# Kernel optimization log

Measured on AMD Instinct MI355X. Metric: run time of the kernel, lower is better.

## Reference

```python
import jax, jax.numpy as jnp
import numpy as np

E = 16      # number of encoders
L = 3       # RNN blocks per encoder
D_IN = 32   # input feature dim
D = 512     # RNN state dim
H_FF = 2048 # encoder FFNN hidden
D_ENC = 512 # encoder output dim
N_DEC = 4   # decoder layers
H_DEC = 2048
D_OUT = 1024
T = 128     # sequence length


def setup_inputs() -> dict:
    key = jax.random.key(0)
    ks = jax.random.split(key, 16)
    def s(k, shape, fan):
        return jax.random.normal(k, shape, jnp.float32) / np.sqrt(fan).astype(np.float32)
    return {
        "x": jax.random.normal(ks[0], (1, T, D_IN), jnp.float32),
        "W_in0": s(ks[1], (E, D_IN, D), D_IN),
        "Wh0": s(ks[2], (E, D, D), D),
        "b0": jnp.zeros((E, D), jnp.float32),
        "W_in_rest": s(ks[3], (E, L - 1, D, D), D),
        "Wh_rest": s(ks[4], (E, L - 1, D, D), D),
        "b_rest": jnp.zeros((E, L - 1, D), jnp.float32),
        "W_ff1": s(ks[5], (E, L * D, H_FF), L * D),
        "b_ff1": jnp.zeros((E, H_FF), jnp.float32),
        "W_ff2": s(ks[6], (E, H_FF, D_ENC), H_FF),
        "b_ff2": jnp.zeros((E, D_ENC), jnp.float32),
        "W_d0": s(ks[7], (E * D_ENC, H_DEC), E * D_ENC),
        "b_d0": jnp.zeros((H_DEC,), jnp.float32),
        "W_dmid": s(ks[8], (N_DEC - 2, H_DEC, H_DEC), H_DEC),
        "b_dmid": jnp.zeros((N_DEC - 2, H_DEC), jnp.float32),
        "W_dout": s(ks[9], (H_DEC, D_OUT), H_DEC),
        "b_dout": jnp.zeros((D_OUT,), jnp.float32),
    }


def reference(x, W_in0, Wh0, b0, W_in_rest, Wh_rest, b_rest,
              W_ff1, b_ff1, W_ff2, b_ff2,
              W_d0, b_d0, W_dmid, b_dmid, W_dout, b_dout):
    def step(h, x_t):
        # h: [E, L, D] stacked-RNN states for all 16 encoders; x_t: [D_IN]
        h0 = jnp.tanh(jnp.einsum('i,eid->ed', x_t, W_in0)
                      + jnp.einsum('ed,edk->ek', h[:, 0], Wh0) + b0)
        hs = [h0]
        for l in range(1, L):  # chain blocks: input = previous block's new state
            hl = jnp.tanh(jnp.einsum('ed,edk->ek', hs[-1], W_in_rest[:, l - 1])
                          + jnp.einsum('ed,edk->ek', h[:, l], Wh_rest[:, l - 1])
                          + b_rest[:, l - 1])
            hs.append(hl)
        h_new = jnp.stack(hs, axis=1)                    # [E, L, D]
        cat = h_new.reshape(E, L * D)                    # cat(states, dim=-1)
        ff = jax.nn.gelu(jnp.einsum('ef,efh->eh', cat, W_ff1) + b_ff1)
        enc_out = jnp.einsum('eh,ehk->ek', ff, W_ff2) + b_ff2  # [E, D_ENC]
        # decoder over concatenated encoder outputs
        z = jnp.tanh(enc_out.reshape(-1) @ W_d0 + b_d0)
        for i in range(N_DEC - 2):
            z = jnp.tanh(z @ W_dmid[i] + b_dmid[i])
        y = z @ W_dout + b_dout                          # [D_OUT]
        return h_new, y

    h_init = jnp.zeros((E, L, D), x.dtype)
    _, ys = jax.lax.scan(step, h_init, x[0])             # [T, D_OUT]
    return ys[None]                                      # [1, T, D_OUT]
```

## Files before the change

kernel.cpp:

```cpp
#include <hip/hip_runtime.h>
#include <hip/hip_bf16.h>
#include <hip/hip_fp16.h>

#define E_ 16
#define T_ 128

typedef _Float16 h2_t __attribute__((ext_vector_type(2)));
typedef _Float16 half4_t __attribute__((ext_vector_type(4)));
typedef _Float16 half8_t __attribute__((ext_vector_type(8)));
typedef float f32x4 __attribute__((ext_vector_type(4)));

__device__ __forceinline__ float fdot2u(uint32_t w, uint32_t h, float acc) {
#if __has_builtin(__builtin_amdgcn_fdot2)
  return __builtin_amdgcn_fdot2(__builtin_bit_cast(h2_t, w),
                                __builtin_bit_cast(h2_t, h), acc, false);
#else
  h2_t wv = __builtin_bit_cast(h2_t, w), hv = __builtin_bit_cast(h2_t, h);
  return acc + (float)wv.x * (float)hv.x + (float)wv.y * (float)hv.y;
#endif
}

__device__ __forceinline__ uint32_t rdlane(uint32_t v, int l) {
  return (uint32_t)__builtin_amdgcn_readlane((int)v, l);
}

__device__ __forceinline__ uint32_t packh2(float a, float b) {
  h2_t p; p.x = (_Float16)a; p.y = (_Float16)b;
  return __builtin_bit_cast(uint32_t, p);
}

__device__ __forceinline__ float apply_act(float v, int act) {
  if (act == 1) return tanhf(v);
  if (act == 2) {
    const float c = 0.7978845608028654f;
    return 0.5f * v * (1.0f + tanhf(c * (v + 0.044715f * v * v * v)));
  }
  return v;
}

template<int NT>
__global__ void __launch_bounds__(256) gemm_mfma(
    const float* __restrict__ A, const float* __restrict__ W,
    const float* __restrict__ bias, float* __restrict__ C, float* __restrict__ part,
    int N, int K, int lda, int ldc,
    long sAe, long sWe, long sBe, long sCe,
    int S, int act)
{
  int n0 = blockIdx.x * (32 * NT);
  int e  = blockIdx.y;
  int s  = blockIdx.z;
  const float* Ae = A + (long)e * sAe;
  const float* We = W + (long)e * sWe;
  int kper = K / S;
  int kb = s * kper, ke2 = kb + kper;

  __shared__ _Float16 As[128 * 40];

  int tid  = threadIdx.x;
  int lane = tid & 63;
  int w    = tid >> 6;
  int wm   = (w >> 1) * 64;
  int wn   = (w & 1) * (16 * NT);
  int l16  = lane & 15;
  int lk   = lane >> 4;

  f32x4 acc[4][NT];
  #pragma unroll
  for (int i = 0; i < 4; ++i)
    #pragma unroll
    for (int j = 0; j < NT; ++j)
      acc[i][j] = (f32x4){0.f, 0.f, 0.f, 0.f};

  for (int k0 = kb; k0 < ke2; k0 += 32) {
    __syncthreads();
    #pragma unroll
    for (int i = 0; i < 4; ++i) {
      int idx = tid + 256 * i;
      int row = idx >> 3, k4 = idx & 7;
      float4 a4 = *(const float4*)(Ae + (long)row * lda + k0 + k4 * 4);
      half4_t hv;
      hv.x = (_Float16)a4.x; hv.y = (_Float16)a4.y;
      hv.z = (_Float16)a4.z; hv.w = (_Float16)a4.w;
      *(half4_t*)(&As[row * 40 + k4 * 4]) = hv;
    }
    __syncthreads();
    #pragma unroll
    for (int nt = 0; nt < NT; ++nt) {
      int ncol = n0 + wn + nt * 16 + l16;
      const float* Wc = We + (long)(k0 + lk * 8) * N + ncol;
      half8_t b;
      #pragma unroll
      for (int j = 0; j < 8; ++j) b[j] = (_Float16)Wc[(long)j * N];
      #pragma unroll
      for (int mt = 0; mt < 4; ++mt) {
        half8_t a = *(const half8_t*)(&As[(wm + mt * 16 + l16) * 40 + lk * 8]);
        acc[mt][nt] = __builtin_amdgcn_mfma_f32_16x16x32_f16(a, b, acc[mt][nt], 0, 0, 0);
      }
    }
  }

  if (S == 1) {
    #pragma unroll
    for (int mt = 0; mt < 4; ++mt)
      #pragma unroll
      for (int nt = 0; nt < NT; ++nt) {
        int col = n0 + wn + nt * 16 + l16;
        float bv = bias[(long)e * sBe + col];
        #pragma unroll
        for (int r = 0; r < 4; ++r) {
          int row = wm + mt * 16 + lk * 4 + r;
          C[(long)e * sCe + (long)row * ldc + col] = apply_act(acc[mt][nt][r] + bv, act);
        }
      }
  } else {
    float* pp = part + ((long)(s * gridDim.y + e) * 128) * N;
    #pragma unroll
    for (int mt = 0; mt < 4; ++mt)
      #pragma unroll
      for (int nt = 0; nt < NT; ++nt) {
        int col = n0 + wn + nt * 16 + l16;
        #pragma unroll
        for (int r = 0; r < 4; ++r) {
          int row = wm + mt * 16 + lk * 4 + r;
          pp[(long)row * N + col] = acc[mt][nt][r];
        }
      }
  }
}

__global__ void __launch_bounds__(256) reduce_ep(
    const float* __restrict__ part, const float* __restrict__ bias, float* __restrict__ C,
    int S, int N, int ldc, long sBe, long sCe, int act, int total, int Eb)
{
  int idx = blockIdx.x * 256 + threadIdx.x;
  if (idx >= total) return;
  int n = idx % N;
  int r = (idx / N) & 127;
  int e = idx / (N * 128);
  long sstride = (long)Eb * 128 * N;
  float v = 0.f;
  for (int s = 0; s < S; ++s) v += part[s * sstride + ((long)e * 128 + r) * N + n];
  v = apply_act(v + bias[(long)e * sBe + n], act);
  C[(long)e * sCe + (long)r * ldc + n] = v;
}

#define RNN_NV 46
#define RNN_NG 9

__global__ void
__attribute__((amdgpu_flat_work_group_size(1024, 1024)))
__attribute__((amdgpu_waves_per_eu(4, 4)))
__attribute__((amdgpu_num_vgpr(128)))
rnn_seq(
    const float* __restrict__ P,
    const float* __restrict__ Wh,
    float* __restrict__ H,
    long sWe)
{
  __shared__ uint32_t lw[RNN_NG * 4096];
  __shared__ uint32_t hbuf[256];
  __shared__ float    red[3 * 512];

  int tid  = threadIdx.x;
  int lane = tid & 63;
  int wid  = tid >> 6;
  int kq   = wid >> 2;
  int colg = wid & 3;
  int c0   = colg * 128 + lane * 2;
  int e    = blockIdx.x;

  const float* W = Wh + (long)e * sWe;

  uint32_t w0[RNN_NV], w1[RNN_NV];
  #pragma unroll
  for (int q = 0; q < RNN_NV; ++q) {
    int k = kq * 128 + 2 * q;
    float2 ra = *(const float2*)(W + (long)k * 512 + c0);
    float2 rb = *(const float2*)(W + (long)(k + 1) * 512 + c0);
    w0[q] = packh2(ra.x, rb.x);
    w1[q] = packh2(ra.y, rb.y);
  }
  for (int g = 0; g < RNN_NG; ++g) {
    int k = kq * 128 + 2 * (RNN_NV + 2 * g);
    float2 ra = *(const float2*)(W + (long)(k + 0) * 512 + c0);
    float2 rb = *(const float2*)(W + (long)(k + 1) * 512 + c0);
    float2 rc = *(const float2*)(W + (long)(k + 2) * 512 + c0);
    float2 rd = *(const float2*)(W + (long)(k + 3) * 512 + c0);
    uint4 v;
    v.x = packh2(ra.x, rb.x);
    v.y = packh2(ra.y, rb.y);
    v.z = packh2(rc.x, rd.x);
    v.w = packh2(rc.y, rd.y);
    *(uint4*)(lw + ((long)g * 1024 + tid) * 4) = v;
  }
  if (tid < 256) hbuf[tid] = 0;
  __syncthreads();

  for (int t = 0; t < T_; ++t) {
    float2 pv = make_float2(0.f, 0.f);
    if (kq == 0) pv = *(const float2*)(P + ((long)t * E_ + e) * 512 + c0);
    uint32_t hr = hbuf[kq * 64 + lane];
    float a0 = 0.f, a1 = 0.f;
    #pragma unroll
    for (int q = 0; q < RNN_NV; ++q) {
      uint32_t hb = rdlane(hr, q);
      a0 = fdot2u(w0[q], hb, a0);
      a1 = fdot2u(w1[q], hb, a1);
    }
    #pragma unroll
    for (int g = 0; g < RNN_NG; ++g) {
      uint4 v = *(const uint4*)(lw + (g * 1024 + tid) * 4);
      uint32_t hb0 = rdlane(hr, RNN_NV + 2 * g);
      uint32_t hb1 = rdlane(hr, RNN_NV + 2 * g + 1);
      a0 = fdot2u(v.x, hb0, a0);
      a1 = fdot2u(v.y, hb0, a1);
      a0 = fdot2u(v.z, hb1, a0);
      a1 = fdot2u(v.w, hb1, a1);
    }
    if (kq) *(float2*)(red + (kq - 1) * 512 + c0) = make_float2(a0, a1);
    __syncthreads();
    if (kq == 0) {
      float v0 = a0 + red[c0]     + red[512 + c0]     + red[1024 + c0]     + pv.x;
      float v1 = a1 + red[c0 + 1] + red[512 + c0 + 1] + red[1024 + c0 + 1] + pv.y;
      v0 = tanhf(v0); v1 = tanhf(v1);
      *(float2*)(H + ((long)t * E_ + e) * 1536 + c0) = make_float2(v0, v1);
      hbuf[colg * 64 + lane] = packh2(v0, v1);
    }
    __syncthreads();
  }
}

extern "C" void kernel_launch(void* const* d_in, const int* in_sizes, int n_in,
                              void* d_out, int out_size, void* d_ws, size_t ws_size,
                              hipStream_t stream)
{
  const float* x      = (const float*)d_in[0];
  const float* W_in0  = (const float*)d_in[1];
  const float* Wh0    = (const float*)d_in[2];
  const float* b0     = (const float*)d_in[3];
  const float* W_inr  = (const float*)d_in[4];
  const float* Wh_r   = (const float*)d_in[5];
  const float* b_r    = (const float*)d_in[6];
  const float* W_ff1  = (const float*)d_in[7];
  const float* b_ff1  = (const float*)d_in[8];
  const float* W_ff2  = (const float*)d_in[9];
  const float* b_ff2  = (const float*)d_in[10];
  const float* W_d0   = (const float*)d_in[11];
  const float* b_d0   = (const float*)d_in[12];
  const float* W_dmid = (const float*)d_in[13];
  const float* b_dmid = (const float*)d_in[14];
  const float* W_dout = (const float*)d_in[15];
  const float* b_dout = (const float*)d_in[16];
  float* ws = (float*)d_ws;

  float* h    = ws;
  float* P    = ws + 3145728;
  float* FF   = ws + 4194304;
  float* ENC  = ws + 8388608;
  float* Z0   = ws + 9437184;
  float* Z1   = ws + 9699328;
  float* Z2   = ws + 9961472;
  float* PART = ws + 10223616;

  (void)in_sizes; (void)n_in; (void)out_size; (void)ws_size;

  dim3 blk(256);

  gemm_mfma<2><<<dim3(8,16,1), blk, 0, stream>>>(x, W_in0, b0, P, PART,
      512, 32, 32, 8192, 0L, 16384L, 512L, 512L, 1, 0);
  rnn_seq<<<dim3(16), dim3(1024), 0, stream>>>(P, Wh0, h, 262144L);
  gemm_mfma<1><<<dim3(16,16,1), blk, 0, stream>>>(h, W_inr, b_r, P, PART,
      512, 512, 24576, 8192, 1536L, 524288L, 1024L, 512L, 1, 0);
  rnn_seq<<<dim3(16), dim3(1024), 0, stream>>>(P, Wh_r, h + 512, 524288L);
  gemm_mfma<1><<<dim3(16,16,1), blk, 0, stream>>>(h + 512, W_inr + 262144, b_r + 512, P, PART,
      512, 512, 24576, 8192, 1536L, 524288L, 1024L, 512L, 1, 0);
  rnn_seq<<<dim3(16), dim3(1024), 0, stream>>>(P, Wh_r + 262144, h + 1024, 524288L);
  gemm_mfma<2><<<dim3(32,16,1), blk, 0, stream>>>(h, W_ff1, b_ff1, FF, PART,
      2048, 1536, 24576, 32768, 1536L, 3145728L, 2048L, 2048L, 1, 2);
  gemm_mfma<1><<<dim3(16,16,2), blk, 0, stream>>>(FF, W_ff2, b_ff2, ENC, PART,
      512, 2048, 32768, 8192, 2048L, 1048576L, 512L, 512L, 2, 0);
  reduce_ep<<<dim3(4096), blk, 0, stream>>>(PART, b_ff2, ENC,
      2, 512, 8192, 512L, 512L, 0, 16*128*512, 16);
  gemm_mfma<2><<<dim3(32,1,8), blk, 0, stream>>>(ENC, W_d0, b_d0, Z0, PART,
      2048, 8192, 8192, 2048, 0L, 0L, 0L, 0L, 8, 0);
  reduce_ep<<<dim3(1024), blk, 0, stream>>>(PART, b_d0, Z0,
      8, 2048, 2048, 0L, 0L, 1, 128*2048, 1);
  gemm_mfma<2><<<dim3(32,1,8), blk, 0, stream>>>(Z0, W_dmid, b_dmid, Z1, PART,
      2048, 2048, 2048, 2048, 0L, 0L, 0L, 0L, 8, 0);
  reduce_ep<<<dim3(1024), blk, 0, stream>>>(PART, b_dmid, Z1,
      8, 2048, 2048, 0L, 0L, 1, 128*2048, 1);
  gemm_mfma<2><<<dim3(32,1,8), blk, 0, stream>>>(Z1, W_dmid + 4194304, b_dmid + 2048, Z2, PART,
      2048, 2048, 2048, 2048, 0L, 0L, 0L, 0L, 8, 0);
  reduce_ep<<<dim3(1024), blk, 0, stream>>>(PART, b_dmid + 2048, Z2,
      8, 2048, 2048, 0L, 0L, 1, 128*2048, 1);
  gemm_mfma<1><<<dim3(32,1,8), blk, 0, stream>>>(Z2, W_dout, b_dout, (float*)d_out, PART,
      1024, 2048, 2048, 1024, 0L, 0L, 0L, 0L, 8, 0);
  reduce_ep<<<dim3(512), blk, 0, stream>>>(PART, b_dout, (float*)d_out,
      8, 1024, 1024, 0L, 0L, 0, 128*1024, 1);
}
```

Baseline: 1.203 ms.

## Store part of RNN recurrent weights in AGPRs instead of VGPRs

Each thread's register-resident slice of the recurrent weight matrix is rearranged: 10 pairs stay in VGPRs, 9 LDS groups are kept, and 36 pairs move into accumulation registers (AGPRs) through inline asm accvgpr write/read. The forced waves_per_eu and num_vgpr limits are dropped, so the compiler can use the unified VGPR+AGPR file. The aim is to relieve VGPR pressure and spilling at 1024 threads per block while keeping the weights on chip. The cost is an extra accvgpr_read before every fdot2 pair in the per-step loop, plus the risk that the compiler's register allocation or occupancy changes.

```diff
diff --git a/kernel.cpp b/kernel.cpp
--- a/kernel.cpp
+++ b/kernel.cpp
@@ -144,13 +144,50 @@
   C[(long)e * sCe + (long)r * ldc + n] = v;
 }
 
-#define RNN_NV 46
+#define RNN_QR 10
 #define RNN_NG 9
+#define RNN_AGQ0 28
+
+#define AG_DECL(j) uint32_t ag##j##_0, ag##j##_1, ag##j##_2, ag##j##_3, \
+                            ag##j##_4, ag##j##_5, ag##j##_6, ag##j##_7
+#define AG_WRITE(x, var) asm volatile("v_accvgpr_write_b32 %0, %1" : "=a"(var) : "v"(x))
+#define AG_READ(var, tmp) asm volatile("v_accvgpr_read_b32 %0, %1" : "=v"(tmp) : "a"(var))
+
+#define AG_PACK1(q, va, vb) do { \
+    int k_ = kq * 128 + 2 * (q); \
+    float2 ra_ = *(const float2*)(W + (long)k_ * 512 + c0); \
+    float2 rb_ = *(const float2*)(W + (long)(k_ + 1) * 512 + c0); \
+    uint32_t u0_ = packh2(ra_.x, rb_.x); \
+    uint32_t u1_ = packh2(ra_.y, rb_.y); \
+    AG_WRITE(u0_, va); \
+    AG_WRITE(u1_, vb); \
+  } while (0)
+
+#define AG_PACK4(j, qb) do { \
+    AG_PACK1((qb) + 0, ag##j##_0, ag##j##_1); \
+    AG_PACK1((qb) + 1, ag##j##_2, ag##j##_3); \
+    AG_PACK1((qb) + 2, ag##j##_4, ag##j##_5); \
+    AG_PACK1((qb) + 3, ag##j##_6, ag##j##_7); \
+  } while (0)
+
+#define AG_DOT1(q, va, vb) do { \
+    uint32_t hb_ = rdlane(hr, (q)); \
+    uint32_t t0_, t1_; \
+    AG_READ(va, t0_); \
+    AG_READ(vb, t1_); \
+    a0 = fdot2u(t0_, hb_, a0); \
+    a1 = fdot2u(t1_, hb_, a1); \
+  } while (0)
+
+#define AG_DOT4(j, qb) do { \
+    AG_DOT1((qb) + 0, ag##j##_0, ag##j##_1); \
+    AG_DOT1((qb) + 1, ag##j##_2, ag##j##_3); \
+    AG_DOT1((qb) + 2, ag##j##_4, ag##j##_5); \
+    AG_DOT1((qb) + 3, ag##j##_6, ag##j##_7); \
+  } while (0)
 
 __global__ void
 __attribute__((amdgpu_flat_work_group_size(1024, 1024)))
-__attribute__((amdgpu_waves_per_eu(4, 4)))
-__attribute__((amdgpu_num_vgpr(128)))
 rnn_seq(
     const float* __restrict__ P,
     const float* __restrict__ Wh,
@@ -171,9 +208,12 @@
 
   const float* W = Wh + (long)e * sWe;
 
-  uint32_t w0[RNN_NV], w1[RNN_NV];
+  AG_DECL(0); AG_DECL(1); AG_DECL(2); AG_DECL(3); AG_DECL(4);
+  AG_DECL(5); AG_DECL(6); AG_DECL(7); AG_DECL(8);
+
+  uint32_t w0[RNN_QR], w1[RNN_QR];
   #pragma unroll
-  for (int q = 0; q < RNN_NV; ++q) {
+  for (int q = 0; q < RNN_QR; ++q) {
     int k = kq * 128 + 2 * q;
     float2 ra = *(const float2*)(W + (long)k * 512 + c0);
     float2 rb = *(const float2*)(W + (long)(k + 1) * 512 + c0);
@@ -181,7 +221,7 @@
     w1[q] = packh2(ra.y, rb.y);
   }
   for (int g = 0; g < RNN_NG; ++g) {
-    int k = kq * 128 + 2 * (RNN_NV + 2 * g);
+    int k = kq * 128 + 2 * (RNN_QR + 2 * g);
     float2 ra = *(const float2*)(W + (long)(k + 0) * 512 + c0);
     float2 rb = *(const float2*)(W + (long)(k + 1) * 512 + c0);
     float2 rc = *(const float2*)(W + (long)(k + 2) * 512 + c0);
@@ -193,6 +233,16 @@
     v.w = packh2(rc.y, rd.y);
     *(uint4*)(lw + ((long)g * 1024 + tid) * 4) = v;
   }
+  AG_PACK4(0, RNN_AGQ0 + 0);
+  AG_PACK4(1, RNN_AGQ0 + 4);
+  AG_PACK4(2, RNN_AGQ0 + 8);
+  AG_PACK4(3, RNN_AGQ0 + 12);
+  AG_PACK4(4, RNN_AGQ0 + 16);
+  AG_PACK4(5, RNN_AGQ0 + 20);
+  AG_PACK4(6, RNN_AGQ0 + 24);
+  AG_PACK4(7, RNN_AGQ0 + 28);
+  AG_PACK4(8, RNN_AGQ0 + 32);
+
   if (tid < 256) hbuf[tid] = 0;
   __syncthreads();
 
@@ -202,7 +252,7 @@
     uint32_t hr = hbuf[kq * 64 + lane];
     float a0 = 0.f, a1 = 0.f;
     #pragma unroll
-    for (int q = 0; q < RNN_NV; ++q) {
+    for (int q = 0; q < RNN_QR; ++q) {
       uint32_t hb = rdlane(hr, q);
       a0 = fdot2u(w0[q], hb, a0);
       a1 = fdot2u(w1[q], hb, a1);
@@ -210,13 +260,23 @@
     #pragma unroll
     for (int g = 0; g < RNN_NG; ++g) {
       uint4 v = *(const uint4*)(lw + (g * 1024 + tid) * 4);
-      uint32_t hb0 = rdlane(hr, RNN_NV + 2 * g);
-      uint32_t hb1 = rdlane(hr, RNN_NV + 2 * g + 1);
+      uint32_t hb0 = rdlane(hr, RNN_QR + 2 * g);
+      uint32_t hb1 = rdlane(hr, RNN_QR + 2 * g + 1);
       a0 = fdot2u(v.x, hb0, a0);
       a1 = fdot2u(v.y, hb0, a1);
       a0 = fdot2u(v.z, hb1, a0);
       a1 = fdot2u(v.w, hb1, a1);
     }
+    AG_DOT4(0, RNN_AGQ0 + 0);
+    AG_DOT4(1, RNN_AGQ0 + 4);
+    AG_DOT4(2, RNN_AGQ0 + 8);
+    AG_DOT4(3, RNN_AGQ0 + 12);
+    AG_DOT4(4, RNN_AGQ0 + 16);
+    AG_DOT4(5, RNN_AGQ0 + 20);
+    AG_DOT4(6, RNN_AGQ0 + 24);
+    AG_DOT4(7, RNN_AGQ0 + 28);
+    AG_DOT4(8, RNN_AGQ0 + 32);
+
     if (kq) *(float2*)(red + (kq - 1) * 512 + c0) = make_float2(a0, a1);
     __syncthreads();
     if (kq == 0) {
```

New measurement: 1.343 ms. 1.12x slower.

## Rewrite RNN recurrence matvec with MFMA and per-wave column ownership

Applied to the files above, without the earlier changes.

The sequential RNN kernel now computes the hidden-state matvec with 16x16x32 f16 MFMA instructions. Each wave owns 32 output columns across the full K, so the cross-wave reduction buffer and one partial-sum pass are gone. Weights are split between AGPR/VGPR fragments and LDS. The cost is heavy redundancy: the state vector is broadcast to all 16 rows of the A operand and only row 0 of each output tile is used. The intent is lower per-step latency on the serial critical path.

```diff
diff --git a/kernel.cpp b/kernel.cpp
--- a/kernel.cpp
+++ b/kernel.cpp
@@ -9,25 +9,6 @@
 typedef _Float16 half4_t __attribute__((ext_vector_type(4)));
 typedef _Float16 half8_t __attribute__((ext_vector_type(8)));
 typedef float f32x4 __attribute__((ext_vector_type(4)));
-
-__device__ __forceinline__ float fdot2u(uint32_t w, uint32_t h, float acc) {
-#if __has_builtin(__builtin_amdgcn_fdot2)
-  return __builtin_amdgcn_fdot2(__builtin_bit_cast(h2_t, w),
-                                __builtin_bit_cast(h2_t, h), acc, false);
-#else
-  h2_t wv = __builtin_bit_cast(h2_t, w), hv = __builtin_bit_cast(h2_t, h);
-  return acc + (float)wv.x * (float)hv.x + (float)wv.y * (float)hv.y;
-#endif
-}
-
-__device__ __forceinline__ uint32_t rdlane(uint32_t v, int l) {
-  return (uint32_t)__builtin_amdgcn_readlane((int)v, l);
-}
-
-__device__ __forceinline__ uint32_t packh2(float a, float b) {
-  h2_t p; p.x = (_Float16)a; p.y = (_Float16)b;
-  return __builtin_bit_cast(uint32_t, p);
-}
 
 __device__ __forceinline__ float apply_act(float v, int act) {
   if (act == 1) return tanhf(v);
@@ -144,87 +125,98 @@
   C[(long)e * sCe + (long)r * ldc + n] = v;
 }
 
-#define RNN_NV 46
-#define RNN_NG 9
-
 __global__ void
 __attribute__((amdgpu_flat_work_group_size(1024, 1024)))
-__attribute__((amdgpu_waves_per_eu(4, 4)))
-__attribute__((amdgpu_num_vgpr(128)))
 rnn_seq(
     const float* __restrict__ P,
     const float* __restrict__ Wh,
     float* __restrict__ H,
     long sWe)
 {
-  __shared__ uint32_t lw[RNN_NG * 4096];
-  __shared__ uint32_t hbuf[256];
-  __shared__ float    red[3 * 512];
+  __shared__ half8_t lwB[9 * 16 * 64];
+  __shared__ _Float16 hbuf[512];
 
   int tid  = threadIdx.x;
   int lane = tid & 63;
-  int wid  = tid >> 6;
-  int kq   = wid >> 2;
-  int colg = wid & 3;
-  int c0   = colg * 128 + lane * 2;
+  int w    = tid >> 6;
+  int l16  = lane & 15;
+  int lk   = lane >> 4;
   int e    = blockIdx.x;
+  int colbase = w * 32;
 
   const float* W = Wh + (long)e * sWe;
 
-  uint32_t w0[RNN_NV], w1[RNN_NV];
-  #pragma unroll
-  for (int q = 0; q < RNN_NV; ++q) {
-    int k = kq * 128 + 2 * q;
-    float2 ra = *(const float2*)(W + (long)k * 512 + c0);
-    float2 rb = *(const float2*)(W + (long)(k + 1) * 512 + c0);
-    w0[q] = packh2(ra.x, rb.x);
-    w1[q] = packh2(ra.y, rb.y);
-  }
-  for (int g = 0; g < RNN_NG; ++g) {
-    int k = kq * 128 + 2 * (RNN_NV + 2 * g);
-    float2 ra = *(const float2*)(W + (long)(k + 0) * 512 + c0);
-    float2 rb = *(const float2*)(W + (long)(k + 1) * 512 + c0);
-    float2 rc = *(const float2*)(W + (long)(k + 2) * 512 + c0);
-    float2 rd = *(const float2*)(W + (long)(k + 3) * 512 + c0);
-    uint4 v;
-    v.x = packh2(ra.x, rb.x);
-    v.y = packh2(ra.y, rb.y);
-    v.z = packh2(rc.x, rd.x);
-    v.w = packh2(rc.y, rd.y);
-    *(uint4*)(lw + ((long)g * 1024 + tid) * 4) = v;
-  }
-  if (tid < 256) hbuf[tid] = 0;
+  auto loadfrag = [&](int ct, int kt) -> half8_t {
+    const float* Wc = W + (long)(kt * 32 + lk * 8) * 512 + colbase + ct * 16 + l16;
+    half8_t b;
+    #pragma unroll
+    for (int j = 0; j < 8; ++j) b[j] = (_Float16)Wc[(long)j * 512];
+    return b;
+  };
+
+  half8_t ba0[8], ba1[8];
+  #pragma unroll
+  for (int kt = 0; kt < 8; ++kt) {
+    ba0[kt] = loadfrag(0, kt); asm("" : "+a"(ba0[kt]));
+    ba1[kt] = loadfrag(1, kt); asm("" : "+a"(ba1[kt]));
+  }
+  half8_t bv0[4], bv1[3];
+  #pragma unroll
+  for (int i = 0; i < 4; ++i) bv0[i] = loadfrag(0, 8 + i);
+  #pragma unroll
+  for (int i = 0; i < 3; ++i) bv1[i] = loadfrag(1, 8 + i);
+  for (int s = 0; s < 9; ++s) {
+    int ct = (s < 4) ? 0 : 1;
+    int kt = (s < 4) ? (12 + s) : (s + 7);
+    lwB[(s * 16 + w) * 64 + lane] = loadfrag(ct, kt);
+  }
+  if (tid < 256) ((uint32_t*)hbuf)[tid] = 0;
   __syncthreads();
 
   for (int t = 0; t < T_; ++t) {
-    float2 pv = make_float2(0.f, 0.f);
-    if (kq == 0) pv = *(const float2*)(P + ((long)t * E_ + e) * 512 + c0);
-    uint32_t hr = hbuf[kq * 64 + lane];
-    float a0 = 0.f, a1 = 0.f;
-    #pragma unroll
-    for (int q = 0; q < RNN_NV; ++q) {
-      uint32_t hb = rdlane(hr, q);
-      a0 = fdot2u(w0[q], hb, a0);
-      a1 = fdot2u(w1[q], hb, a1);
-    }
-    #pragma unroll
-    for (int g = 0; g < RNN_NG; ++g) {
-      uint4 v = *(const uint4*)(lw + (g * 1024 + tid) * 4);
-      uint32_t hb0 = rdlane(hr, RNN_NV + 2 * g);
-      uint32_t hb1 = rdlane(hr, RNN_NV + 2 * g + 1);
-      a0 = fdot2u(v.x, hb0, a0);
-      a1 = fdot2u(v.y, hb0, a1);
-      a0 = fdot2u(v.z, hb1, a0);
-      a1 = fdot2u(v.w, hb1, a1);
-    }
-    if (kq) *(float2*)(red + (kq - 1) * 512 + c0) = make_float2(a0, a1);
-    __syncthreads();
-    if (kq == 0) {
-      float v0 = a0 + red[c0]     + red[512 + c0]     + red[1024 + c0]     + pv.x;
-      float v1 = a1 + red[c0 + 1] + red[512 + c0 + 1] + red[1024 + c0 + 1] + pv.y;
-      v0 = tanhf(v0); v1 = tanhf(v1);
-      *(float2*)(H + ((long)t * E_ + e) * 1536 + c0) = make_float2(v0, v1);
-      hbuf[colg * 64 + lane] = packh2(v0, v1);
+    float p0 = 0.f, p1 = 0.f;
+    if (lane < 16) {
+      const float* Pp = P + ((long)t * E_ + e) * 512 + colbase + lane;
+      p0 = Pp[0]; p1 = Pp[16];
+    }
+    f32x4 acc0 = {0.f, 0.f, 0.f, 0.f}, acc1 = {0.f, 0.f, 0.f, 0.f};
+    #pragma unroll
+    for (int kt = 0; kt < 8; ++kt) {
+      half8_t a = *(const half8_t*)(&hbuf[kt * 32 + lk * 8]);
+      acc0 = __builtin_amdgcn_mfma_f32_16x16x32_f16(a, ba0[kt], acc0, 0, 0, 0);
+      acc1 = __builtin_amdgcn_mfma_f32_16x16x32_f16(a, ba1[kt], acc1, 0, 0, 0);
+    }
+    #pragma unroll
+    for (int i = 0; i < 4; ++i) {
+      int kt = 8 + i;
+      half8_t a = *(const half8_t*)(&hbuf[kt * 32 + lk * 8]);
+      acc0 = __builtin_amdgcn_mfma_f32_16x16x32_f16(a, bv0[i], acc0, 0, 0, 0);
+      if (i < 3)
+        acc1 = __builtin_amdgcn_mfma_f32_16x16x32_f16(a, bv1[i], acc1, 0, 0, 0);
+    }
+    {
+      half8_t a = *(const half8_t*)(&hbuf[11 * 32 + lk * 8]);
+      half8_t b = lwB[(4 * 16 + w) * 64 + lane];
+      acc1 = __builtin_amdgcn_mfma_f32_16x16x32_f16(a, b, acc1, 0, 0, 0);
+    }
+    #pragma unroll
+    for (int i = 0; i < 4; ++i) {
+      int kt = 12 + i;
+      half8_t a  = *(const half8_t*)(&hbuf[kt * 32 + lk * 8]);
+      half8_t b0 = lwB[(i * 16 + w) * 64 + lane];
+      half8_t b1 = lwB[((5 + i) * 16 + w) * 64 + lane];
+      acc0 = __builtin_amdgcn_mfma_f32_16x16x32_f16(a, b0, acc0, 0, 0, 0);
+      acc1 = __builtin_amdgcn_mfma_f32_16x16x32_f16(a, b1, acc1, 0, 0, 0);
+    }
+    __syncthreads();
+    if (lane < 16) {
+      float v0 = tanhf(acc0[0] + p0);
+      float v1 = tanhf(acc1[0] + p1);
+      int col = colbase + lane;
+      float* Hp = H + ((long)t * E_ + e) * 1536;
+      Hp[col] = v0; Hp[col + 16] = v1;
+      hbuf[col] = (_Float16)v0;
+      hbuf[col + 16] = (_Float16)v1;
     }
     __syncthreads();
   }
```

After: 1.575 ms. +30.9%, slower.

## Restructure RNN recurrence to one column per thread with AGPR-resident weights

Applied to the files above, without the earlier changes.

The recurrent kernel moves from 1024 threads, each holding two columns over a quarter of K, to 512 threads, each owning one output column over all of K. This removes the cross-wave LDS reduction and one of the two barriers' worth of work per timestep. To hold the full 512x1 column of fp16 weights, each thread splits it across three places: regular VGPRs, AccVGPRs written and read through inline asm, and LDS. The risk is fewer waves to hide latency, plus extra accvgpr read instructions in the inner loop.

```diff
diff --git a/kernel.cpp b/kernel.cpp
--- a/kernel.cpp
+++ b/kernel.cpp
@@ -144,88 +144,110 @@
   C[(long)e * sCe + (long)r * ldc + n] = v;
 }
 
-#define RNN_NV 46
-#define RNN_NG 9
+#define RW_NVL 24
+#define RW_AL0 24
+#define RW_LL0 48
+
+#define AG_DECL(j) uint32_t ag##j##_0, ag##j##_1, ag##j##_2, ag##j##_3, \
+                            ag##j##_4, ag##j##_5, ag##j##_6, ag##j##_7
+#define AG_W(x, var) asm volatile("v_accvgpr_write_b32 %0, %1" : "=a"(var) : "v"(x))
+#define AG_R(var, tmp) asm volatile("v_accvgpr_read_b32 %0, %1" : "=v"(tmp) : "a"(var))
+#define AG_PACKQ(q, var) do { \
+    uint32_t u_ = packh2(W[(long)(2 * (q)) * 512], W[(long)(2 * (q) + 1) * 512]); \
+    AG_W(u_, var); } while (0)
+#define AG_PACK8(j, Lb) do { \
+    AG_PACKQ(4 * (Lb) + 0, ag##j##_0); AG_PACKQ(4 * (Lb) + 1, ag##j##_1); \
+    AG_PACKQ(4 * (Lb) + 2, ag##j##_2); AG_PACKQ(4 * (Lb) + 3, ag##j##_3); \
+    AG_PACKQ(4 * (Lb) + 4, ag##j##_4); AG_PACKQ(4 * (Lb) + 5, ag##j##_5); \
+    AG_PACKQ(4 * (Lb) + 6, ag##j##_6); AG_PACKQ(4 * (Lb) + 7, ag##j##_7); } while (0)
+#define AG_DOT8(j, Lb) do { \
+    uint32_t t_; \
+    uint32_t h0_ = rdlane(hr.x, (Lb)), h1_ = rdlane(hr.y, (Lb)); \
+    uint32_t h2_ = rdlane(hr.z, (Lb)), h3_ = rdlane(hr.w, (Lb)); \
+    AG_R(ag##j##_0, t_); a0 = fdot2u(t_, h0_, a0); \
+    AG_R(ag##j##_1, t_); a1 = fdot2u(t_, h1_, a1); \
+    AG_R(ag##j##_2, t_); a2 = fdot2u(t_, h2_, a2); \
+    AG_R(ag##j##_3, t_); a3 = fdot2u(t_, h3_, a3); \
+    h0_ = rdlane(hr.x, (Lb) + 1); h1_ = rdlane(hr.y, (Lb) + 1); \
+    h2_ = rdlane(hr.z, (Lb) + 1); h3_ = rdlane(hr.w, (Lb) + 1); \
+    AG_R(ag##j##_4, t_); a0 = fdot2u(t_, h0_, a0); \
+    AG_R(ag##j##_5, t_); a1 = fdot2u(t_, h1_, a1); \
+    AG_R(ag##j##_6, t_); a2 = fdot2u(t_, h2_, a2); \
+    AG_R(ag##j##_7, t_); a3 = fdot2u(t_, h3_, a3); } while (0)
 
 __global__ void
-__attribute__((amdgpu_flat_work_group_size(1024, 1024)))
-__attribute__((amdgpu_waves_per_eu(4, 4)))
-__attribute__((amdgpu_num_vgpr(128)))
+__attribute__((amdgpu_flat_work_group_size(512, 512)))
+__attribute__((amdgpu_waves_per_eu(2, 2)))
 rnn_seq(
     const float* __restrict__ P,
     const float* __restrict__ Wh,
     float* __restrict__ H,
     long sWe)
 {
-  __shared__ uint32_t lw[RNN_NG * 4096];
+  __shared__ uint32_t lw[16 * 512 * 4];
   __shared__ uint32_t hbuf[256];
-  __shared__ float    red[3 * 512];
 
   int tid  = threadIdx.x;
   int lane = tid & 63;
-  int wid  = tid >> 6;
-  int kq   = wid >> 2;
-  int colg = wid & 3;
-  int c0   = colg * 128 + lane * 2;
   int e    = blockIdx.x;
 
-  const float* W = Wh + (long)e * sWe;
-
-  uint32_t w0[RNN_NV], w1[RNN_NV];
+  const float* W = Wh + (long)e * sWe + tid;
+
+  AG_DECL(0); AG_DECL(1); AG_DECL(2);  AG_DECL(3);  AG_DECL(4);  AG_DECL(5);
+  AG_DECL(6); AG_DECL(7); AG_DECL(8);  AG_DECL(9);  AG_DECL(10); AG_DECL(11);
+
+  uint32_t wv[RW_NVL * 4];
   #pragma unroll
-  for (int q = 0; q < RNN_NV; ++q) {
-    int k = kq * 128 + 2 * q;
-    float2 ra = *(const float2*)(W + (long)k * 512 + c0);
-    float2 rb = *(const float2*)(W + (long)(k + 1) * 512 + c0);
-    w0[q] = packh2(ra.x, rb.x);
-    w1[q] = packh2(ra.y, rb.y);
-  }
-  for (int g = 0; g < RNN_NG; ++g) {
-    int k = kq * 128 + 2 * (RNN_NV + 2 * g);
-    float2 ra = *(const float2*)(W + (long)(k + 0) * 512 + c0);
-    float2 rb = *(const float2*)(W + (long)(k + 1) * 512 + c0);
-    float2 rc = *(const float2*)(W + (long)(k + 2) * 512 + c0);
-    float2 rd = *(const float2*)(W + (long)(k + 3) * 512 + c0);
+  for (int q = 0; q < RW_NVL * 4; ++q)
+    wv[q] = packh2(W[(long)(2 * q) * 512], W[(long)(2 * q + 1) * 512]);
+  AG_PACK8(0,  RW_AL0 + 0);  AG_PACK8(1,  RW_AL0 + 2);
+  AG_PACK8(2,  RW_AL0 + 4);  AG_PACK8(3,  RW_AL0 + 6);
+  AG_PACK8(4,  RW_AL0 + 8);  AG_PACK8(5,  RW_AL0 + 10);
+  AG_PACK8(6,  RW_AL0 + 12); AG_PACK8(7,  RW_AL0 + 14);
+  AG_PACK8(8,  RW_AL0 + 16); AG_PACK8(9,  RW_AL0 + 18);
+  AG_PACK8(10, RW_AL0 + 20); AG_PACK8(11, RW_AL0 + 22);
+  for (int g = 0; g < 16; ++g) {
+    int q0 = 4 * (RW_LL0 + g);
     uint4 v;
-    v.x = packh2(ra.x, rb.x);
-    v.y = packh2(ra.y, rb.y);
-    v.z = packh2(rc.x, rd.x);
-    v.w = packh2(rc.y, rd.y);
-    *(uint4*)(lw + ((long)g * 1024 + tid) * 4) = v;
+    v.x = packh2(W[(long)(2 * (q0 + 0)) * 512], W[(long)(2 * (q0 + 0) + 1) * 512]);
+    v.y = packh2(W[(long)(2 * (q0 + 1)) * 512], W[(long)(2 * (q0 + 1) + 1) * 512]);
+    v.z = packh2(W[(long)(2 * (q0 + 2)) * 512], W[(long)(2 * (q0 + 2) + 1) * 512]);
+    v.w = packh2(W[(long)(2 * (q0 + 3)) * 512], W[(long)(2 * (q0 + 3) + 1) * 512]);
+    *(uint4*)(lw + ((long)g * 512 + tid) * 4) = v;
   }
   if (tid < 256) hbuf[tid] = 0;
   __syncthreads();
 
   for (int t = 0; t < T_; ++t) {
-    float2 pv = make_float2(0.f, 0.f);
-    if (kq == 0) pv = *(const float2*)(P + ((long)t * E_ + e) * 512 + c0);
-    uint32_t hr = hbuf[kq * 64 + lane];
-    float a0 = 0.f, a1 = 0.f;
-    #pragma unroll
-    for (int q = 0; q < RNN_NV; ++q) {
-      uint32_t hb = rdlane(hr, q);
-      a0 = fdot2u(w0[q], hb, a0);
-      a1 = fdot2u(w1[q], hb, a1);
+    float p = P[((long)t * E_ + e) * 512 + tid];
+    uint4 hr = *(const uint4*)(hbuf + lane * 4);
+    float a0 = 0.f, a1 = 0.f, a2 = 0.f, a3 = 0.f;
+    #pragma unroll
+    for (int L = 0; L < RW_NVL; ++L) {
+      a0 = fdot2u(wv[4 * L + 0], rdlane(hr.x, L), a0);
+      a1 = fdot2u(wv[4 * L + 1], rdlane(hr.y, L), a1);
+      a2 = fdot2u(wv[4 * L + 2], rdlane(hr.z, L), a2);
+      a3 = fdot2u(wv[4 * L + 3], rdlane(hr.w, L), a3);
     }
-    #pragma unroll
-    for (int g = 0; g < RNN_NG; ++g) {
-      uint4 v = *(const uint4*)(lw + (g * 1024 + tid) * 4);
-      uint32_t hb0 = rdlane(hr, RNN_NV + 2 * g);
-      uint32_t hb1 = rdlane(hr, RNN_NV + 2 * g + 1);
-      a0 = fdot2u(v.x, hb0, a0);
-      a1 = fdot2u(v.y, hb0, a1);
-      a0 = fdot2u(v.z, hb1, a0);
-      a1 = fdot2u(v.w, hb1, a1);
+    AG_DOT8(0,  RW_AL0 + 0);  AG_DOT8(1,  RW_AL0 + 2);
+    AG_DOT8(2,  RW_AL0 + 4);  AG_DOT8(3,  RW_AL0 + 6);
+    AG_DOT8(4,  RW_AL0 + 8);  AG_DOT8(5,  RW_AL0 + 10);
+    AG_DOT8(6,  RW_AL0 + 12); AG_DOT8(7,  RW_AL0 + 14);
+    AG_DOT8(8,  RW_AL0 + 16); AG_DOT8(9,  RW_AL0 + 18);
+    AG_DOT8(10, RW_AL0 + 20); AG_DOT8(11, RW_AL0 + 22);
+    #pragma unroll
+    for (int g = 0; g < 16; ++g) {
+      uint4 v = *(const uint4*)(lw + (g * 512 + tid) * 4);
+      int L = RW_LL0 + g;
+      a0 = fdot2u(v.x, rdlane(hr.x, L), a0);
+      a1 = fdot2u(v.y, rdlane(hr.y, L), a1);
+      a2 = fdot2u(v.z, rdlane(hr.z, L), a2);
+      a3 = fdot2u(v.w, rdlane(hr.w, L), a3);
     }
-    if (kq) *(float2*)(red + (kq - 1) * 512 + c0) = make_float2(a0, a1);
     __syncthreads();
-    if (kq == 0) {
-      float v0 = a0 + red[c0]     + red[512 + c0]     + red[1024 + c0]     + pv.x;
-      float v1 = a1 + red[c0 + 1] + red[512 + c0 + 1] + red[1024 + c0 + 1] + pv.y;
-      v0 = tanhf(v0); v1 = tanhf(v1);
-      *(float2*)(H + ((long)t * E_ + e) * 1536 + c0) = make_float2(v0, v1);
-      hbuf[colg * 64 + lane] = packh2(v0, v1);
-    }
+    float v0 = tanhf((a0 + a1) + (a2 + a3) + p);
+    H[((long)t * E_ + e) * 1536 + tid] = v0;
+    ((_Float16*)hbuf)[tid] = (_Float16)v0;
     __syncthreads();
   }
 }
@@ -268,13 +290,13 @@
 
   gemm_mfma<2><<<dim3(8,16,1), blk, 0, stream>>>(x, W_in0, b0, P, PART,
       512, 32, 32, 8192, 0L, 16384L, 512L, 512L, 1, 0);
-  rnn_seq<<<dim3(16), dim3(1024), 0, stream>>>(P, Wh0, h, 262144L);
+  rnn_seq<<<dim3(16), dim3(512), 0, stream>>>(P, Wh0, h, 262144L);
   gemm_mfma<1><<<dim3(16,16,1), blk, 0, stream>>>(h, W_inr, b_r, P, PART,
       512, 512, 24576, 8192, 1536L, 524288L, 1024L, 512L, 1, 0);
-  rnn_seq<<<dim3(16), dim3(1024), 0, stream>>>(P, Wh_r, h + 512, 524288L);
+  rnn_seq<<<dim3(16), dim3(512), 0, stream>>>(P, Wh_r, h + 512, 524288L);
   gemm_mfma<1><<<dim3(16,16,1), blk, 0, stream>>>(h + 512, W_inr + 262144, b_r + 512, P, PART,
       512, 512, 24576, 8192, 1536L, 524288L, 1024L, 512L, 1, 0);
-  rnn_seq<<<dim3(16), dim3(1024), 0, stream>>>(P, Wh_r + 262144, h + 1024, 524288L);
+  rnn_seq<<<dim3(16), dim3(512), 0, stream>>>(P, Wh_r + 262144, h + 1024, 524288L);
   gemm_mfma<2><<<dim3(32,16,1), blk, 0, stream>>>(h, W_ff1, b_ff1, FF, PART,
       2048, 1536, 24576, 32768, 1536L, 3145728L, 2048L, 2048L, 1, 2);
   gemm_mfma<1><<<dim3(16,16,2), blk, 0, stream>>>(FF, W_ff2, b_ff2, ENC, PART,
```

Measured after the change: 1.627 ms. 1.35x slower.
